# Optimization experiments

Hardware: AMD Instinct MI355X
Metric: run time of the kernel (lower is better)

The kernel has to match this reference:

```python
import jax, jax.numpy as jnp
import numpy as np

NUM_KEYS = 128          # int(sqrt(num_cdmoe_experts)) = sqrt(16384)
TOP_K = 8               # num_cdmoe_experts_per_head
NUM_HEADS = 4           # num_cdmoe_heads


def setup_inputs() -> dict:
    key = jax.random.key(0)
    ks = jax.random.split(key, 8)
    b, t, d = 1, 2048, 1024
    inter = 2048
    E, h, ret = 16384, NUM_HEADS, 64
    s = 0.02
    return {
        "hidden_states": jax.random.normal(ks[0], (b, t, d), jnp.float32),
        "w_queries": jax.random.normal(ks[1], (h * ret, d), jnp.float32) * s,
        "keys": jax.random.normal(ks[2], (h, NUM_KEYS, 2, ret // 2), jnp.float32) * s,
        "down_embed": jax.random.normal(ks[3], (E, d), jnp.float32) * s,
        "up_embed": jax.random.normal(ks[4], (E, d), jnp.float32) * s,
        "w_gate": jax.random.normal(ks[5], (inter, d), jnp.float32) * s,
        "w_up": jax.random.normal(ks[6], (inter, d), jnp.float32) * s,
        "w_down": jax.random.normal(ks[7], (d, inter), jnp.float32) * s,
    }


def reference(hidden_states, w_queries, keys, down_embed, up_embed, w_gate, w_up, w_down):
    b, t, d = hidden_states.shape
    h, nk, _, n = keys.shape  # (heads, num_keys, 2, retrieval_dim//2)
    k = TOP_K

    # query projection, split into the two product-key halves: (b, t, 2, h, n)
    q = (hidden_states @ w_queries.T).reshape(b, t, 2, h, n)
    # sim: (2, b, t, h, num_keys)
    sim = jnp.einsum("btphn,hkpn->pbthk", q, keys)

    # per-codebook top-k
    sx, ix = jax.lax.top_k(sim[0], k)  # (b, t, h, k)
    sy, iy = jax.lax.top_k(sim[1], k)

    # cartesian combine: (b, t, h, k*k)
    all_scores = (sx[..., :, None] + sy[..., None, :]).reshape(b, t, h, k * k)
    all_idx = (ix[..., :, None] * nk + iy[..., None, :]).reshape(b, t, h, k * k)

    scores, pos = jax.lax.top_k(all_scores, k)          # (b, t, h, k)
    indices = jnp.take_along_axis(all_idx, pos, axis=-1)  # expert ids in [0, nk*nk)

    de = down_embed[indices]  # (b, t, h, k, d)
    ue = up_embed[indices]    # (b, t, h, k, d)

    ew = jnp.einsum("btd,bthkd->bthk", hidden_states, de)
    ew = jax.nn.silu(ew) * jax.nn.softmax(scores, axis=-1)
    experts_states = jnp.einsum("bthk,bthkd->btd", ew, ue)

    # dense (inherited DogeMLP) path
    mlp = (jax.nn.silu(hidden_states @ w_gate.T) * (hidden_states @ w_up.T)) @ w_down.T
    return mlp + experts_states
```

## Files before the change

### kernel.cpp

```cpp
#include <hip/hip_runtime.h>
#include <hip/hip_bf16.h>
#include <math.h>


#define TOKENS 2048
#define DIM    1024
#define INTER  2048
#define NKEYS  128
#define TOPK   8
#define HEADS  4
#define NINF  -3.4e38f

typedef unsigned short ushort_t;
typedef __attribute__((ext_vector_type(8))) short bf16x8;
typedef __attribute__((ext_vector_type(4))) float f32x4;

__device__ __forceinline__ float bf2f(ushort_t u) {
    unsigned int x = (unsigned int)u << 16;
    float f; __builtin_memcpy(&f, &x, 4); return f;
}
__device__ __forceinline__ ushort_t f2bf_rne(float f) {
    unsigned int x; __builtin_memcpy(&x, &f, 4);
    x += 0x7fffu + ((x >> 16) & 1u);
    return (ushort_t)(x >> 16);
}
__device__ __forceinline__ void gload_lds16(const void* g, void* l) {
    __builtin_amdgcn_global_load_lds(
        (const __attribute__((address_space(1))) unsigned int*)g,
        (__attribute__((address_space(3))) unsigned int*)l, 16, 0, 0);
}

__global__ __launch_bounds__(256) void convert_all(
    const float* __restrict__ h,  const float* __restrict__ wq,
    const float* __restrict__ wg, const float* __restrict__ wu,
    const float* __restrict__ wd,
    ushort_t* __restrict__ hb,  ushort_t* __restrict__ wqb,
    ushort_t* __restrict__ wgb, ushort_t* __restrict__ wub,
    ushort_t* __restrict__ wdb) {
    const int i = blockIdx.x * 256 + threadIdx.x;
    const float* src; ushort_t* dst; int off;
    if      (i <  262144) { src = h;  dst = hb;  off = i; }
    else if (i <  294912) { src = wq; dst = wqb; off = i - 262144; }
    else if (i <  557056) { src = wg; dst = wgb; off = i - 294912; }
    else if (i <  819200) { src = wu; dst = wub; off = i - 557056; }
    else                  { src = wd; dst = wdb; off = i - 819200; }
    const float4* p = (const float4*)src + (size_t)off * 2;
    const float4 a = p[0], b = p[1];
    uint4 o;
    o.x = (unsigned)f2bf_rne(a.x) | ((unsigned)f2bf_rne(a.y) << 16);
    o.y = (unsigned)f2bf_rne(a.z) | ((unsigned)f2bf_rne(a.w) << 16);
    o.z = (unsigned)f2bf_rne(b.x) | ((unsigned)f2bf_rne(b.y) << 16);
    o.w = (unsigned)f2bf_rne(b.z) | ((unsigned)f2bf_rne(b.w) << 16);
    ((uint4*)dst)[off] = o;
}

template<int BM, int BN, int WR, int WC, int FM, int FN, int EPI>
__global__ __launch_bounds__(256) void mfma_gemm(const ushort_t* __restrict__ A,
                                                 const ushort_t* __restrict__ B,
                                                 const void* __restrict__ extra,
                                                 void* __restrict__ Cout,
                                                 int M, int N, int K) {
    static_assert(WR * WC == 4 && WR * FM * 16 == BM && WC * FN * 16 == BN, "geom");
    __shared__ ushort_t As[BM * 32];
    __shared__ ushort_t Bs[BN * 32];
    const int tid = threadIdx.x;
    const int w = tid >> 6, lane = tid & 63;
    const int wr = w / WC, wc = w % WC;
    const int m0 = blockIdx.y * BM, n0 = blockIdx.x * BN;

    const int srow = (w << 4) + (lane >> 2);
    const int scol = (lane & 3) << 3;
    const ushort_t* Ag = &A[(size_t)(m0 + srow) * K + scol];
    const ushort_t* Bg = &B[(size_t)(n0 + srow) * K + scol];
    ushort_t* Al = &As[w << 9];
    ushort_t* Bl = &Bs[w << 9];

    const int frow = lane & 15;
    const int fcol = (lane >> 4) << 3;
    const ushort_t* Afr = &As[(size_t)(wr * FM * 16 + frow) * 32 + fcol];
    const ushort_t* Bfr = &Bs[(size_t)(wc * FN * 16 + frow) * 32 + fcol];

    f32x4 acc[FM][FN];
#pragma unroll
    for (int i = 0; i < FM; ++i)
#pragma unroll
        for (int j = 0; j < FN; ++j) acc[i][j] = (f32x4){0.f, 0.f, 0.f, 0.f};

    for (int k0 = 0; k0 < K; k0 += 32) {
        __syncthreads();
#pragma unroll
        for (int i = 0; i < BM / 64; ++i)
            gload_lds16(Ag + (size_t)i * 64 * K + k0, Al + i * 2048);
#pragma unroll
        for (int i = 0; i < BN / 64; ++i)
            gload_lds16(Bg + (size_t)i * 64 * K + k0, Bl + i * 2048);
        __syncthreads();

        bf16x8 af[FM], bfv[FN];
#pragma unroll
        for (int i = 0; i < FM; ++i) af[i] = *(const bf16x8*)(Afr + i * 512);
#pragma unroll
        for (int j = 0; j < FN; ++j) bfv[j] = *(const bf16x8*)(Bfr + j * 512);
#pragma unroll
        for (int i = 0; i < FM; ++i)
#pragma unroll
            for (int j = 0; j < FN; ++j)
                acc[i][j] = __builtin_amdgcn_mfma_f32_16x16x32_bf16(
                    af[i], bfv[j], acc[i][j], 0, 0, 0);
    }

    const int crow0 = m0 + wr * FM * 16 + ((lane >> 4) << 2);
    const int ccol0 = n0 + wc * FN * 16 + (lane & 15);
#pragma unroll
    for (int i = 0; i < FM; ++i)
#pragma unroll
        for (int j = 0; j < FN; ++j)
#pragma unroll
            for (int r = 0; r < 4; ++r) {
                const size_t off = (size_t)(crow0 + i * 16 + r) * N + ccol0 + j * 16;
                float v = acc[i][j][r];
                if (EPI == 1) {
                    const float gg = bf2f(((const ushort_t*)extra)[off]);
                    v *= gg / (1.f + __expf(-gg));
                    ((ushort_t*)Cout)[off] = f2bf_rne(v);
                } else if (EPI == 2) {
                    ((float*)Cout)[off] = v + ((const float*)extra)[off];
                } else if (EPI == 3) {
                    ((ushort_t*)Cout)[off] = f2bf_rne(v);
                } else {
                    ((float*)Cout)[off] = v;
                }
            }
}

__global__ __launch_bounds__(256) void silu_mul_inplace(const ushort_t* __restrict__ g,
                                                        ushort_t* __restrict__ u) {
    const int i = blockIdx.x * 256 + threadIdx.x;
    const uint4 gv = ((const uint4*)g)[i];
    const uint4 uv = ((const uint4*)u)[i];
    const unsigned gw[4] = {gv.x, gv.y, gv.z, gv.w};
    const unsigned uw[4] = {uv.x, uv.y, uv.z, uv.w};
    unsigned ow[4];
#pragma unroll
    for (int j = 0; j < 4; ++j) {
        const float g0 = bf2f((ushort_t)(gw[j] & 0xffff));
        const float g1 = bf2f((ushort_t)(gw[j] >> 16));
        const float u0 = bf2f((ushort_t)(uw[j] & 0xffff));
        const float u1 = bf2f((ushort_t)(uw[j] >> 16));
        const float v0 = g0 / (1.f + __expf(-g0)) * u0;
        const float v1 = g1 / (1.f + __expf(-g1)) * u1;
        ow[j] = (unsigned)f2bf_rne(v0) | ((unsigned)f2bf_rne(v1) << 16);
    }
    ((uint4*)u)[i] = (uint4){ow[0], ow[1], ow[2], ow[3]};
}

__global__ __launch_bounds__(256) void topk_kernel(const float* __restrict__ q,
                                                   const float* __restrict__ keys,
                                                   int* __restrict__ eidx,
                                                   float* __restrict__ ewgt) {
    const int t = blockIdx.x;
    const int head = threadIdx.x >> 6;
    const int lane = threadIdx.x & 63;

    const float4* qx = (const float4*)&q[(size_t)t * 256 + head * 32];
    const float4* qy = (const float4*)&q[(size_t)t * 256 + 128 + head * 32];
    float4 qxv[8], qyv[8];
#pragma unroll
    for (int n = 0; n < 8; ++n) { qxv[n] = qx[n]; qyv[n] = qy[n]; }

    float cx0, cx1, cy0, cy1;
    {
        float s[4];
#pragma unroll
        for (int j = 0; j < 2; ++j) {
            const int k = 2 * lane + j;
            const float4* kx = (const float4*)&keys[(size_t)(((head << 7) | k) * 2 + 0) * 32];
            const float4* ky = (const float4*)&keys[(size_t)(((head << 7) | k) * 2 + 1) * 32];
            float sx = 0.f, sy = 0.f;
#pragma unroll
            for (int n = 0; n < 8; ++n) {
                const float4 a = qxv[n], b = kx[n];
                sx += a.x * b.x + a.y * b.y + a.z * b.z + a.w * b.w;
                const float4 c = qyv[n], d = ky[n];
                sy += c.x * d.x + c.y * d.y + c.z * d.z + c.w * d.w;
            }
            s[j * 2] = sx; s[j * 2 + 1] = sy;
        }
        cx0 = s[0]; cy0 = s[1]; cx1 = s[2]; cy1 = s[3];
    }

    float sx_mine = NINF, sy_mine = NINF;
    int sxi_mine = 0, syi_mine = 0;
    {
        float c0 = cx0, c1 = cx1;
#pragma unroll
        for (int it = 0; it < TOPK; ++it) {
            float bv; int bi;
            if (c1 > c0) { bv = c1; bi = 2 * lane + 1; } else { bv = c0; bi = 2 * lane; }
#pragma unroll
            for (int m = 1; m < 64; m <<= 1) {
                const float ov = __shfl_xor(bv, m);
                const int   oi = __shfl_xor(bi, m);
                if (ov > bv || (ov == bv && oi < bi)) { bv = ov; bi = oi; }
            }
            if (lane == it) { sx_mine = bv; sxi_mine = bi; }
            if (bi == 2 * lane) c0 = NINF;
            else if (bi == 2 * lane + 1) c1 = NINF;
        }
    }
    {
        float c0 = cy0, c1 = cy1;
#pragma unroll
        for (int it = 0; it < TOPK; ++it) {
            float bv; int bi;
            if (c1 > c0) { bv = c1; bi = 2 * lane + 1; } else { bv = c0; bi = 2 * lane; }
#pragma unroll
            for (int m = 1; m < 64; m <<= 1) {
                const float ov = __shfl_xor(bv, m);
                const int   oi = __shfl_xor(bi, m);
                if (ov > bv || (ov == bv && oi < bi)) { bv = ov; bi = oi; }
            }
            if (lane == it) { sy_mine = bv; syi_mine = bi; }
            if (bi == 2 * lane) c0 = NINF;
            else if (bi == 2 * lane + 1) c1 = NINF;
        }
    }

    const float sa = __shfl(sx_mine, lane >> 3);
    const int   ia = __shfl(sxi_mine, lane >> 3);
    const float sb = __shfl(sy_mine, lane & 7);
    const int   ib = __shfl(syi_mine, lane & 7);
    float cv = sa + sb;
    const int ci = ia * NKEYS + ib;

    float fs_mine = NINF; int fi_mine = 0;
#pragma unroll
    for (int it = 0; it < TOPK; ++it) {
        float bv = cv; int bp = lane; int bx = ci;
#pragma unroll
        for (int m = 1; m < 64; m <<= 1) {
            const float ov = __shfl_xor(bv, m);
            const int   op = __shfl_xor(bp, m);
            const int   ox = __shfl_xor(bx, m);
            if (ov > bv || (ov == bv && op < bp)) { bv = ov; bp = op; bx = ox; }
        }
        if (lane == it) { fs_mine = bv; fi_mine = bx; }
        if (lane == bp) cv = NINF;
    }

    float f[8];
#pragma unroll
    for (int j = 0; j < 8; ++j) f[j] = __shfl(fs_mine, j);
    float mx = f[0];
#pragma unroll
    for (int j = 1; j < 8; ++j) mx = fmaxf(mx, f[j]);
    float ssum = 0.f;
#pragma unroll
    for (int j = 0; j < 8; ++j) ssum += expf(f[j] - mx);
    if (lane < 8) {
        eidx[t * 32 + head * 8 + lane] = fi_mine;
        ewgt[t * 32 + head * 8 + lane] = expf(fs_mine - mx) / ssum;
    }
}

__global__ __launch_bounds__(256) void fused3_kernel(
    const ushort_t* __restrict__ A,  const ushort_t* __restrict__ Bgate,
    const ushort_t* __restrict__ Bup, ushort_t* __restrict__ G,
    ushort_t* __restrict__ U,
    const float* __restrict__ hs, const float* __restrict__ down_embed,
    const float* __restrict__ up_embed, const int* __restrict__ eidx,
    const float* __restrict__ ewgt, float* __restrict__ estate) {
    __shared__ __align__(16) char smem[16896];
    const int b = blockIdx.x;
    const int tid = threadIdx.x;
    const int w = tid >> 6, lane = tid & 63;
    const int r6 = b % 6;

    if (r6 == 2 || r6 == 5) {
        const ushort_t* B = (r6 == 2) ? Bgate : Bup;
        ushort_t*      C  = (r6 == 2) ? G : U;
        const int id = b / 6;
        const int m0 = (id >> 4) * 64, n0 = (id & 15) * 128;
        const int N = INTER, K = DIM;
        ushort_t* As = (ushort_t*)smem;
        ushort_t* Bs = (ushort_t*)(smem + 4096);
        const int wc = w;
        const int srow = (w << 4) + (lane >> 2);
        const int scol = (lane & 3) << 3;
        const ushort_t* Ag = &A[(size_t)(m0 + srow) * K + scol];
        const ushort_t* Bg = &B[(size_t)(n0 + srow) * K + scol];
        ushort_t* Al = &As[w << 9];
        ushort_t* Bl = &Bs[w << 9];
        const int frow = lane & 15;
        const int fcol = (lane >> 4) << 3;
        const ushort_t* Afr = &As[(size_t)frow * 32 + fcol];
        const ushort_t* Bfr = &Bs[(size_t)(wc * 32 + frow) * 32 + fcol];

        f32x4 acc[4][2];
#pragma unroll
        for (int i = 0; i < 4; ++i)
#pragma unroll
            for (int j = 0; j < 2; ++j) acc[i][j] = (f32x4){0.f, 0.f, 0.f, 0.f};

        for (int k0 = 0; k0 < K; k0 += 32) {
            __syncthreads();
            gload_lds16(Ag + k0, Al);
#pragma unroll
            for (int i = 0; i < 2; ++i)
                gload_lds16(Bg + (size_t)i * 64 * K + k0, Bl + i * 2048);
            __syncthreads();

            bf16x8 af[4], bfv[2];
#pragma unroll
            for (int i = 0; i < 4; ++i) af[i] = *(const bf16x8*)(Afr + i * 512);
#pragma unroll
            for (int j = 0; j < 2; ++j) bfv[j] = *(const bf16x8*)(Bfr + j * 512);
#pragma unroll
            for (int i = 0; i < 4; ++i)
#pragma unroll
                for (int j = 0; j < 2; ++j)
                    acc[i][j] = __builtin_amdgcn_mfma_f32_16x16x32_bf16(
                        af[i], bfv[j], acc[i][j], 0, 0, 0);
        }

        const int crow0 = m0 + ((lane >> 4) << 2);
        const int ccol0 = n0 + wc * 32 + (lane & 15);
#pragma unroll
        for (int i = 0; i < 4; ++i)
#pragma unroll
            for (int j = 0; j < 2; ++j)
#pragma unroll
                for (int r = 0; r < 4; ++r) {
                    const size_t off = (size_t)(crow0 + i * 16 + r) * N + ccol0 + j * 16;
                    C[off] = f2bf_rne(acc[i][j][r]);
                }
    } else {
        const int t = (b / 6) * 4 + r6 - (r6 > 2 ? 1 : 0);
        float4 (*partial)[256] = (float4(*)[256])smem;
        int*   eid = (int*)(smem + 16384);
        float* wl  = (float*)(smem + 16512);

        if (tid < 32) { eid[tid] = eidx[t * 32 + tid]; wl[tid] = ewgt[t * 32 + tid]; }

        const float4* hs4 = (const float4*)hs + (size_t)t * 256;
        float4 h[4];
#pragma unroll
        for (int i = 0; i < 4; ++i) h[i] = hs4[i * 64 + lane];

        const float4* de4 = (const float4*)down_embed;
        const float4* ue4 = (const float4*)up_embed;
        __syncthreads();

        float4 acc[4];
#pragma unroll
        for (int i = 0; i < 4; ++i) acc[i] = (float4){0.f, 0.f, 0.f, 0.f};

        float4 d[4], u[4], nd[4], nu[4];
        {
            const size_t bb = (size_t)eid[w * 8] * 256;
#pragma unroll
            for (int i = 0; i < 4; ++i) { d[i] = de4[bb + i * 64 + lane]; u[i] = ue4[bb + i * 64 + lane]; }
        }
#pragma unroll
        for (int jj = 0; jj < 8; ++jj) {
            if (jj < 7) {
                const size_t bb = (size_t)eid[w * 8 + jj + 1] * 256;
#pragma unroll
                for (int i = 0; i < 4; ++i) { nd[i] = de4[bb + i * 64 + lane]; nu[i] = ue4[bb + i * 64 + lane]; }
            }
            float s = 0.f;
#pragma unroll
            for (int i = 0; i < 4; ++i)
                s += h[i].x * d[i].x + h[i].y * d[i].y + h[i].z * d[i].z + h[i].w * d[i].w;
#pragma unroll
            for (int m = 1; m < 64; m <<= 1) s += __shfl_xor(s, m);
            const float c = (s / (1.f + __expf(-s))) * wl[w * 8 + jj];
#pragma unroll
            for (int i = 0; i < 4; ++i) {
                acc[i].x += c * u[i].x; acc[i].y += c * u[i].y;
                acc[i].z += c * u[i].z; acc[i].w += c * u[i].w;
            }
            if (jj < 7) {
#pragma unroll
                for (int i = 0; i < 4; ++i) { d[i] = nd[i]; u[i] = nu[i]; }
            }
        }

#pragma unroll
        for (int i = 0; i < 4; ++i) partial[w][i * 64 + lane] = acc[i];
        __syncthreads();

        const float4 p0 = partial[0][tid], p1 = partial[1][tid];
        const float4 p2 = partial[2][tid], p3 = partial[3][tid];
        float4 o;
        o.x = p0.x + p1.x + p2.x + p3.x;
        o.y = p0.y + p1.y + p2.y + p3.y;
        o.z = p0.z + p1.z + p2.z + p3.z;
        o.w = p0.w + p1.w + p2.w + p3.w;
        ((float4*)estate)[(size_t)t * 256 + tid] = o;
    }
}

extern "C" void kernel_launch(void* const* d_in, const int* in_sizes, int n_in,
                              void* d_out, int out_size, void* d_ws, size_t ws_size,
                              hipStream_t stream) {
    (void)in_sizes; (void)n_in; (void)out_size; (void)ws_size;
    const float* hidden = (const float*)d_in[0];
    const float* wq     = (const float*)d_in[1];
    const float* keys   = (const float*)d_in[2];
    const float* down_e = (const float*)d_in[3];
    const float* up_e   = (const float*)d_in[4];
    const float* wgate  = (const float*)d_in[5];
    const float* wup    = (const float*)d_in[6];
    const float* wdown  = (const float*)d_in[7];
    float* out = (float*)d_out;
    char* ws = (char*)d_ws;

    ushort_t* hb  = (ushort_t*)(ws);
    ushort_t* wqb = (ushort_t*)(ws + (4u << 20));
    ushort_t* wgb = (ushort_t*)(ws + (4608u << 10));
    ushort_t* wub = (ushort_t*)(ws + (8704u << 10));
    ushort_t* wdb = (ushort_t*)(ws + (12800u << 10));
    float*    q   = (float*)   (ws + (16896u << 10));
    ushort_t* act = (ushort_t*)(ws + (18944u << 10));
    ushort_t* g   = (ushort_t*)(ws + (27136u << 10));
    float*    wgt = (float*)   (ws + (35328u << 10));
    int*     eidx = (int*)     (ws + (35584u << 10));
    float* estate = out;

    convert_all<<<4224, 256, 0, stream>>>(hidden, wq, wgate, wup, wdown,
                                          hb, wqb, wgb, wub, wdb);

    mfma_gemm<64, 64, 2, 2, 2, 2, 0><<<dim3(4, 32), 256, 0, stream>>>(
        hb, wqb, nullptr, q, TOKENS, 256, DIM);
    topk_kernel<<<TOKENS, 256, 0, stream>>>(q, keys, eidx, wgt);
    fused3_kernel<<<3072, 256, 0, stream>>>(
        hb, wgb, wub, g, act, hidden, down_e, up_e, eidx, wgt, estate);
    silu_mul_inplace<<<2048, 256, 0, stream>>>(g, act);
    mfma_gemm<64, 64, 2, 2, 2, 2, 2><<<dim3(16, 32), 256, 0, stream>>>(
        act, wdb, estate, out, TOKENS, DIM, INTER);
}
```

Measured before the change: 204.6 us.

## Quantize expert embedding tables to fp8 and split top-k into rank-based kernels

```diff
diff --git a/kernel.cpp b/kernel.cpp
--- a/kernel.cpp
+++ b/kernel.cpp
@@ -9,11 +9,11 @@
 #define NKEYS  128
 #define TOPK   8
 #define HEADS  4
-#define NINF  -3.4e38f
 
 typedef unsigned short ushort_t;
 typedef __attribute__((ext_vector_type(8))) short bf16x8;
 typedef __attribute__((ext_vector_type(4))) float f32x4;
+typedef __attribute__((ext_vector_type(2))) float f32x2;
 
 __device__ __forceinline__ float bf2f(ushort_t u) {
     unsigned int x = (unsigned int)u << 16;
@@ -54,6 +54,23 @@
     ((uint4*)dst)[off] = o;
 }
 
+__global__ __launch_bounds__(256) void conv_tables(
+    const float* __restrict__ de_f32, const float* __restrict__ ue_f32,
+    unsigned* __restrict__ deb, unsigned* __restrict__ ueb) {
+    const int id = blockIdx.x;
+    const float* src = (id < 8192) ? de_f32 : ue_f32;
+    unsigned*    dst = (id < 8192) ? deb : ueb;
+    const size_t eoff = (size_t)(id & 8191) * 2048 + threadIdx.x * 8;
+    const float4* p = (const float4*)(src + eoff);
+    const float4 a = p[0], b = p[1];
+    int w0 = 0, w1 = 0;
+    w0 = __builtin_amdgcn_cvt_pk_fp8_f32(a.x * 64.f, a.y * 64.f, w0, false);
+    w0 = __builtin_amdgcn_cvt_pk_fp8_f32(a.z * 64.f, a.w * 64.f, w0, true);
+    w1 = __builtin_amdgcn_cvt_pk_fp8_f32(b.x * 64.f, b.y * 64.f, w1, false);
+    w1 = __builtin_amdgcn_cvt_pk_fp8_f32(b.z * 64.f, b.w * 64.f, w1, true);
+    *(uint2*)((char*)dst + eoff) = (uint2){(unsigned)w0, (unsigned)w1};
+}
+
 template<int BM, int BN, int WR, int WC, int FM, int FN, int EPI>
 __global__ __launch_bounds__(256) void mfma_gemm(const ushort_t* __restrict__ A,
                                                  const ushort_t* __restrict__ B,
@@ -119,11 +136,7 @@
             for (int r = 0; r < 4; ++r) {
                 const size_t off = (size_t)(crow0 + i * 16 + r) * N + ccol0 + j * 16;
                 float v = acc[i][j][r];
-                if (EPI == 1) {
-                    const float gg = bf2f(((const ushort_t*)extra)[off]);
-                    v *= gg / (1.f + __expf(-gg));
-                    ((ushort_t*)Cout)[off] = f2bf_rne(v);
-                } else if (EPI == 2) {
+                if (EPI == 2) {
                     ((float*)Cout)[off] = v + ((const float*)extra)[off];
                 } else if (EPI == 3) {
                     ((ushort_t*)Cout)[off] = f2bf_rne(v);
@@ -131,6 +144,124 @@
                     ((float*)Cout)[off] = v;
                 }
             }
+}
+
+__global__ __launch_bounds__(256) void sims_f32(const float* __restrict__ q,
+                                                const float* __restrict__ keys,
+                                                float* __restrict__ sims) {
+    const int t = blockIdx.x;
+    const int head = threadIdx.x >> 6;
+    const int lane = threadIdx.x & 63;
+
+    const float4* qx = (const float4*)&q[(size_t)t * 256 + head * 32];
+    const float4* qy = (const float4*)&q[(size_t)t * 256 + 128 + head * 32];
+    float4 qxv[8], qyv[8];
+#pragma unroll
+    for (int n = 0; n < 8; ++n) { qxv[n] = qx[n]; qyv[n] = qy[n]; }
+
+    float s[4];
+#pragma unroll
+    for (int j = 0; j < 2; ++j) {
+        const int k = 2 * lane + j;
+        const float4* kx = (const float4*)&keys[(size_t)(((head << 7) | k) * 2 + 0) * 32];
+        const float4* ky = (const float4*)&keys[(size_t)(((head << 7) | k) * 2 + 1) * 32];
+        float sx = 0.f, sy = 0.f;
+#pragma unroll
+        for (int n = 0; n < 8; ++n) {
+            const float4 a = qxv[n], b = kx[n];
+            sx += a.x * b.x + a.y * b.y + a.z * b.z + a.w * b.w;
+            const float4 c = qyv[n], d = ky[n];
+            sy += c.x * d.x + c.y * d.y + c.z * d.z + c.w * d.w;
+        }
+        s[j * 2] = sx; s[j * 2 + 1] = sy;
+    }
+    float* srow = &sims[(size_t)t * 1024 + head * 256];
+    *(float2*)&srow[2 * lane]       = (float2){s[0], s[2]};
+    *(float2*)&srow[128 + 2 * lane] = (float2){s[1], s[3]};
+}
+
+__global__ __launch_bounds__(256) void topk_select(const float* __restrict__ sims,
+                                                   int* __restrict__ eidx,
+                                                   float* __restrict__ ewgt) {
+    __shared__ float sm[HEADS][256];
+    __shared__ float txv[HEADS][8];
+    __shared__ int   txi[HEADS][8];
+    __shared__ float tyv[HEADS][8];
+    __shared__ int   tyi[HEADS][8];
+    __shared__ float comb[HEADS][64];
+    __shared__ float tfv[HEADS][8];
+    __shared__ int   tfi[HEADS][8];
+    const int t = blockIdx.x;
+    const int head = threadIdx.x >> 6;
+    const int lane = threadIdx.x & 63;
+
+    const float4 v = *(const float4*)&sims[(size_t)t * 1024 + head * 256 + lane * 4];
+    *(float4*)&sm[head][lane * 4] = v;
+
+    const int isY = lane >= 32;
+    const float* base = &sm[head][isY ? 128 : 0];
+    const int gi = (lane * 4) - (isY ? 128 : 0);
+    int r0 = 0, r1 = 0, r2 = 0, r3 = 0;
+#pragma unroll
+    for (int j = 0; j < 128; j += 4) {
+        const float4 sv = *(const float4*)&base[j];
+        r0 += (sv.x > v.x) | ((sv.x == v.x) & (j + 0 < gi + 0));
+        r0 += (sv.y > v.x) | ((sv.y == v.x) & (j + 1 < gi + 0));
+        r0 += (sv.z > v.x) | ((sv.z == v.x) & (j + 2 < gi + 0));
+        r0 += (sv.w > v.x) | ((sv.w == v.x) & (j + 3 < gi + 0));
+        r1 += (sv.x > v.y) | ((sv.x == v.y) & (j + 0 < gi + 1));
+        r1 += (sv.y > v.y) | ((sv.y == v.y) & (j + 1 < gi + 1));
+        r1 += (sv.z > v.y) | ((sv.z == v.y) & (j + 2 < gi + 1));
+        r1 += (sv.w > v.y) | ((sv.w == v.y) & (j + 3 < gi + 1));
+        r2 += (sv.x > v.z) | ((sv.x == v.z) & (j + 0 < gi + 2));
+        r2 += (sv.y > v.z) | ((sv.y == v.z) & (j + 1 < gi + 2));
+        r2 += (sv.z > v.z) | ((sv.z == v.z) & (j + 2 < gi + 2));
+        r2 += (sv.w > v.z) | ((sv.w == v.z) & (j + 3 < gi + 2));
+        r3 += (sv.x > v.w) | ((sv.x == v.w) & (j + 0 < gi + 3));
+        r3 += (sv.y > v.w) | ((sv.y == v.w) & (j + 1 < gi + 3));
+        r3 += (sv.z > v.w) | ((sv.z == v.w) & (j + 2 < gi + 3));
+        r3 += (sv.w > v.w) | ((sv.w == v.w) & (j + 3 < gi + 3));
+    }
+    if (!isY) {
+        if (r0 < TOPK) { txv[head][r0] = v.x; txi[head][r0] = gi + 0; }
+        if (r1 < TOPK) { txv[head][r1] = v.y; txi[head][r1] = gi + 1; }
+        if (r2 < TOPK) { txv[head][r2] = v.z; txi[head][r2] = gi + 2; }
+        if (r3 < TOPK) { txv[head][r3] = v.w; txi[head][r3] = gi + 3; }
+    } else {
+        if (r0 < TOPK) { tyv[head][r0] = v.x; tyi[head][r0] = gi + 0; }
+        if (r1 < TOPK) { tyv[head][r1] = v.y; tyi[head][r1] = gi + 1; }
+        if (r2 < TOPK) { tyv[head][r2] = v.z; tyi[head][r2] = gi + 2; }
+        if (r3 < TOPK) { tyv[head][r3] = v.w; tyi[head][r3] = gi + 3; }
+    }
+
+    const float cv = txv[head][lane >> 3] + tyv[head][lane & 7];
+    const int   ci = txi[head][lane >> 3] * NKEYS + tyi[head][lane & 7];
+    comb[head][lane] = cv;
+
+    int cr = 0;
+#pragma unroll
+    for (int j = 0; j < 64; j += 4) {
+        const float4 sv = *(const float4*)&comb[head][j];
+        cr += (sv.x > cv) | ((sv.x == cv) & (j + 0 < lane));
+        cr += (sv.y > cv) | ((sv.y == cv) & (j + 1 < lane));
+        cr += (sv.z > cv) | ((sv.z == cv) & (j + 2 < lane));
+        cr += (sv.w > cv) | ((sv.w == cv) & (j + 3 < lane));
+    }
+    if (cr < TOPK) { tfv[head][cr] = cv; tfi[head][cr] = ci; }
+
+    float f[8];
+#pragma unroll
+    for (int j = 0; j < 8; ++j) f[j] = tfv[head][j];
+    float mx = f[0];
+#pragma unroll
+    for (int j = 1; j < 8; ++j) mx = fmaxf(mx, f[j]);
+    float ssum = 0.f;
+#pragma unroll
+    for (int j = 0; j < 8; ++j) ssum += expf(f[j] - mx);
+    if (lane < 8) {
+        eidx[t * 32 + head * 8 + lane] = tfi[head][lane];
+        ewgt[t * 32 + head * 8 + lane] = expf(f[lane] - mx) / ssum;
+    }
 }
 
 __global__ __launch_bounds__(256) void silu_mul_inplace(const ushort_t* __restrict__ g,
@@ -154,121 +285,12 @@
     ((uint4*)u)[i] = (uint4){ow[0], ow[1], ow[2], ow[3]};
 }
 
-__global__ __launch_bounds__(256) void topk_kernel(const float* __restrict__ q,
-                                                   const float* __restrict__ keys,
-                                                   int* __restrict__ eidx,
-                                                   float* __restrict__ ewgt) {
-    const int t = blockIdx.x;
-    const int head = threadIdx.x >> 6;
-    const int lane = threadIdx.x & 63;
-
-    const float4* qx = (const float4*)&q[(size_t)t * 256 + head * 32];
-    const float4* qy = (const float4*)&q[(size_t)t * 256 + 128 + head * 32];
-    float4 qxv[8], qyv[8];
-#pragma unroll
-    for (int n = 0; n < 8; ++n) { qxv[n] = qx[n]; qyv[n] = qy[n]; }
-
-    float cx0, cx1, cy0, cy1;
-    {
-        float s[4];
-#pragma unroll
-        for (int j = 0; j < 2; ++j) {
-            const int k = 2 * lane + j;
-            const float4* kx = (const float4*)&keys[(size_t)(((head << 7) | k) * 2 + 0) * 32];
-            const float4* ky = (const float4*)&keys[(size_t)(((head << 7) | k) * 2 + 1) * 32];
-            float sx = 0.f, sy = 0.f;
-#pragma unroll
-            for (int n = 0; n < 8; ++n) {
-                const float4 a = qxv[n], b = kx[n];
-                sx += a.x * b.x + a.y * b.y + a.z * b.z + a.w * b.w;
-                const float4 c = qyv[n], d = ky[n];
-                sy += c.x * d.x + c.y * d.y + c.z * d.z + c.w * d.w;
-            }
-            s[j * 2] = sx; s[j * 2 + 1] = sy;
-        }
-        cx0 = s[0]; cy0 = s[1]; cx1 = s[2]; cy1 = s[3];
-    }
-
-    float sx_mine = NINF, sy_mine = NINF;
-    int sxi_mine = 0, syi_mine = 0;
-    {
-        float c0 = cx0, c1 = cx1;
-#pragma unroll
-        for (int it = 0; it < TOPK; ++it) {
-            float bv; int bi;
-            if (c1 > c0) { bv = c1; bi = 2 * lane + 1; } else { bv = c0; bi = 2 * lane; }
-#pragma unroll
-            for (int m = 1; m < 64; m <<= 1) {
-                const float ov = __shfl_xor(bv, m);
-                const int   oi = __shfl_xor(bi, m);
-                if (ov > bv || (ov == bv && oi < bi)) { bv = ov; bi = oi; }
-            }
-            if (lane == it) { sx_mine = bv; sxi_mine = bi; }
-            if (bi == 2 * lane) c0 = NINF;
-            else if (bi == 2 * lane + 1) c1 = NINF;
-        }
-    }
-    {
-        float c0 = cy0, c1 = cy1;
-#pragma unroll
-        for (int it = 0; it < TOPK; ++it) {
-            float bv; int bi;
-            if (c1 > c0) { bv = c1; bi = 2 * lane + 1; } else { bv = c0; bi = 2 * lane; }
-#pragma unroll
-            for (int m = 1; m < 64; m <<= 1) {
-                const float ov = __shfl_xor(bv, m);
-                const int   oi = __shfl_xor(bi, m);
-                if (ov > bv || (ov == bv && oi < bi)) { bv = ov; bi = oi; }
-            }
-            if (lane == it) { sy_mine = bv; syi_mine = bi; }
-            if (bi == 2 * lane) c0 = NINF;
-            else if (bi == 2 * lane + 1) c1 = NINF;
-        }
-    }
-
-    const float sa = __shfl(sx_mine, lane >> 3);
-    const int   ia = __shfl(sxi_mine, lane >> 3);
-    const float sb = __shfl(sy_mine, lane & 7);
-    const int   ib = __shfl(syi_mine, lane & 7);
-    float cv = sa + sb;
-    const int ci = ia * NKEYS + ib;
-
-    float fs_mine = NINF; int fi_mine = 0;
-#pragma unroll
-    for (int it = 0; it < TOPK; ++it) {
-        float bv = cv; int bp = lane; int bx = ci;
-#pragma unroll
-        for (int m = 1; m < 64; m <<= 1) {
-            const float ov = __shfl_xor(bv, m);
-            const int   op = __shfl_xor(bp, m);
-            const int   ox = __shfl_xor(bx, m);
-            if (ov > bv || (ov == bv && op < bp)) { bv = ov; bp = op; bx = ox; }
-        }
-        if (lane == it) { fs_mine = bv; fi_mine = bx; }
-        if (lane == bp) cv = NINF;
-    }
-
-    float f[8];
-#pragma unroll
-    for (int j = 0; j < 8; ++j) f[j] = __shfl(fs_mine, j);
-    float mx = f[0];
-#pragma unroll
-    for (int j = 1; j < 8; ++j) mx = fmaxf(mx, f[j]);
-    float ssum = 0.f;
-#pragma unroll
-    for (int j = 0; j < 8; ++j) ssum += expf(f[j] - mx);
-    if (lane < 8) {
-        eidx[t * 32 + head * 8 + lane] = fi_mine;
-        ewgt[t * 32 + head * 8 + lane] = expf(fs_mine - mx) / ssum;
-    }
-}
-
 __global__ __launch_bounds__(256) void fused3_kernel(
     const ushort_t* __restrict__ A,  const ushort_t* __restrict__ Bgate,
     const ushort_t* __restrict__ Bup, ushort_t* __restrict__ G,
     ushort_t* __restrict__ U,
-    const float* __restrict__ hs, const float* __restrict__ down_embed,
-    const float* __restrict__ up_embed, const int* __restrict__ eidx,
+    const float* __restrict__ hs, const unsigned* __restrict__ de_tab,
+    const unsigned* __restrict__ ue_tab, const int* __restrict__ eidx,
     const float* __restrict__ ewgt, float* __restrict__ estate) {
     __shared__ __align__(16) char smem[16896];
     const int b = blockIdx.x;
@@ -346,39 +368,42 @@
         float4 h[4];
 #pragma unroll
         for (int i = 0; i < 4; ++i) h[i] = hs4[i * 64 + lane];
-
-        const float4* de4 = (const float4*)down_embed;
-        const float4* ue4 = (const float4*)up_embed;
         __syncthreads();
 
         float4 acc[4];
 #pragma unroll
         for (int i = 0; i < 4; ++i) acc[i] = (float4){0.f, 0.f, 0.f, 0.f};
 
-        float4 d[4], u[4], nd[4], nu[4];
+        unsigned d[4], u[4], nd[4], nu[4];
         {
             const size_t bb = (size_t)eid[w * 8] * 256;
 #pragma unroll
-            for (int i = 0; i < 4; ++i) { d[i] = de4[bb + i * 64 + lane]; u[i] = ue4[bb + i * 64 + lane]; }
+            for (int i = 0; i < 4; ++i) { d[i] = de_tab[bb + i * 64 + lane]; u[i] = ue_tab[bb + i * 64 + lane]; }
         }
 #pragma unroll
         for (int jj = 0; jj < 8; ++jj) {
             if (jj < 7) {
                 const size_t bb = (size_t)eid[w * 8 + jj + 1] * 256;
 #pragma unroll
-                for (int i = 0; i < 4; ++i) { nd[i] = de4[bb + i * 64 + lane]; nu[i] = ue4[bb + i * 64 + lane]; }
+                for (int i = 0; i < 4; ++i) { nd[i] = de_tab[bb + i * 64 + lane]; nu[i] = ue_tab[bb + i * 64 + lane]; }
             }
             float s = 0.f;
 #pragma unroll
-            for (int i = 0; i < 4; ++i)
-                s += h[i].x * d[i].x + h[i].y * d[i].y + h[i].z * d[i].z + h[i].w * d[i].w;
+            for (int i = 0; i < 4; ++i) {
+                const f32x2 lo = __builtin_amdgcn_cvt_pk_f32_fp8((int)d[i], false);
+                const f32x2 hi = __builtin_amdgcn_cvt_pk_f32_fp8((int)d[i], true);
+                s += h[i].x * lo[0] + h[i].y * lo[1] + h[i].z * hi[0] + h[i].w * hi[1];
+            }
 #pragma unroll
             for (int m = 1; m < 64; m <<= 1) s += __shfl_xor(s, m);
-            const float c = (s / (1.f + __expf(-s))) * wl[w * 8 + jj];
+            const float sr = s * 0.015625f;
+            const float c = (sr / (1.f + __expf(-sr))) * wl[w * 8 + jj];
 #pragma unroll
             for (int i = 0; i < 4; ++i) {
-                acc[i].x += c * u[i].x; acc[i].y += c * u[i].y;
-                acc[i].z += c * u[i].z; acc[i].w += c * u[i].w;
+                const f32x2 lo = __builtin_amdgcn_cvt_pk_f32_fp8((int)u[i], false);
+                const f32x2 hi = __builtin_amdgcn_cvt_pk_f32_fp8((int)u[i], true);
+                acc[i].x += c * lo[0]; acc[i].y += c * lo[1];
+                acc[i].z += c * hi[0]; acc[i].w += c * hi[1];
             }
             if (jj < 7) {
 #pragma unroll
@@ -393,10 +418,10 @@
         const float4 p0 = partial[0][tid], p1 = partial[1][tid];
         const float4 p2 = partial[2][tid], p3 = partial[3][tid];
         float4 o;
-        o.x = p0.x + p1.x + p2.x + p3.x;
-        o.y = p0.y + p1.y + p2.y + p3.y;
-        o.z = p0.z + p1.z + p2.z + p3.z;
-        o.w = p0.w + p1.w + p2.w + p3.w;
+        o.x = (p0.x + p1.x + p2.x + p3.x) * 0.015625f;
+        o.y = (p0.y + p1.y + p2.y + p3.y) * 0.015625f;
+        o.z = (p0.z + p1.z + p2.z + p3.z) * 0.015625f;
+        o.w = (p0.w + p1.w + p2.w + p3.w) * 0.015625f;
         ((float4*)estate)[(size_t)t * 256 + tid] = o;
     }
 }
@@ -423,19 +448,23 @@
     ushort_t* wdb = (ushort_t*)(ws + (12800u << 10));
     float*    q   = (float*)   (ws + (16896u << 10));
     ushort_t* act = (ushort_t*)(ws + (18944u << 10));
+    float*   sims = (float*)act;
     ushort_t* g   = (ushort_t*)(ws + (27136u << 10));
     float*    wgt = (float*)   (ws + (35328u << 10));
     int*     eidx = (int*)     (ws + (35584u << 10));
+    unsigned* deb = (unsigned*)(ws + 36700160u);
+    unsigned* ueb = (unsigned*)(ws + 53477376u);
     float* estate = out;
 
     convert_all<<<4224, 256, 0, stream>>>(hidden, wq, wgate, wup, wdown,
                                           hb, wqb, wgb, wub, wdb);
-
+    conv_tables<<<16384, 256, 0, stream>>>(down_e, up_e, deb, ueb);
     mfma_gemm<64, 64, 2, 2, 2, 2, 0><<<dim3(4, 32), 256, 0, stream>>>(
         hb, wqb, nullptr, q, TOKENS, 256, DIM);
-    topk_kernel<<<TOKENS, 256, 0, stream>>>(q, keys, eidx, wgt);
+    sims_f32<<<TOKENS, 256, 0, stream>>>(q, keys, sims);
+    topk_select<<<TOKENS, 256, 0, stream>>>(sims, eidx, wgt);
     fused3_kernel<<<3072, 256, 0, stream>>>(
-        hb, wgb, wub, g, act, hidden, down_e, up_e, eidx, wgt, estate);
+        hb, wgb, wub, g, act, hidden, deb, ueb, eidx, wgt, estate);
     silu_mul_inplace<<<2048, 256, 0, stream>>>(g, act);
     mfma_gemm<64, 64, 2, 2, 2, 2, 2><<<dim3(16, 32), 256, 0, stream>>>(
         act, wdb, estate, out, TOKENS, DIM, INTER);
```

Result: slower. 225.6 us (+10.2%).
